# Kernel optimization log

Hardware: AMD Instinct MI355X
Metric: run time of the kernel (lower is better)

Reference implementation:

```python
import jax, jax.numpy as jnp
import numpy as np

NUM_CLASSES = 20
IOU_T = 0.5
NEG_RATIO = 3.0
VXY = 0.1
VWH = 0.2
EPS16 = 9.765625e-4  # torch.finfo(torch.float16).eps


def ltrb2xywh(b):
    return jnp.concatenate([(b[..., :2] + b[..., 2:]) * 0.5, b[..., 2:] - b[..., :2]], -1)


def xywh2ltrb(b):
    return jnp.concatenate([b[..., :2] - b[..., 2:] * 0.5, b[..., :2] + b[..., 2:] * 0.5], -1)


def pairwise_iou(gb, ab):
    # gb [G,4] ltrb, ab [A,4] ltrb -> [G,A]
    lt = jnp.maximum(gb[:, None, :2], ab[None, :, :2])
    rb = jnp.minimum(gb[:, None, 2:], ab[None, :, 2:])
    wh = jnp.clip(rb - lt, 0.0)
    inter = wh[..., 0] * wh[..., 1]
    area_g = (gb[:, 2] - gb[:, 0]) * (gb[:, 3] - gb[:, 1])
    area_a = (ab[:, 2] - ab[:, 0]) * (ab[:, 3] - ab[:, 1])
    return inter / jnp.clip(area_g[:, None] + area_a[None, :] - inter, 1e-8)


def setup_inputs() -> dict:
    key = jax.random.key(0)
    k = jax.random.split(key, 7)
    B, A, G, C = 64, 8732, 50, NUM_CLASSES + 1
    preg = jax.random.normal(k[0], (B, 4, A), jnp.float32) * 0.1
    pcls = jax.random.normal(k[1], (B, C, A), jnp.float32)
    acxy = jax.random.uniform(k[2], (A, 2), jnp.float32)
    awh = jax.random.uniform(k[3], (A, 2), jnp.float32, 0.05, 0.5)
    ancs_xywh = jnp.concatenate([acxy, awh], -1)
    gcxy = jax.random.uniform(k[4], (B, G, 2), jnp.float32, 0.2, 0.8)
    gwh = jax.random.uniform(k[5], (B, G, 2), jnp.float32, 0.05, 0.4)
    gboxes_ltrb = jnp.concatenate([gcxy - gwh * 0.5, gcxy + gwh * 0.5], -1)
    glabels = jax.random.randint(k[6], (B, G), 0, C)  # 0 == padding/background
    return {"preg": preg, "pcls": pcls, "ancs_xywh": ancs_xywh,
            "gboxes_ltrb": gboxes_ltrb, "glabels": glabels}


def _loss(preg, pcls, ancs_xywh, gboxes_ltrb, glabels):
    B, _, A = preg.shape
    preg_bad = jnp.transpose(preg, (0, 2, 1))  # [B,A,4]
    anc_ltrb = xywh2ltrb(ancs_xywh)

    def match(gb, gl):
        iou = pairwise_iou(gb, anc_ltrb)                    # [G,A]
        iou = jnp.where((gl > 0)[:, None], iou, -1.0)       # mask padded gts
        return jnp.argmax(iou, 0), jnp.max(iou, 0) >= IOU_T  # best gt per anchor, pos mask

    boxes_index, mask_pos = jax.vmap(match)(gboxes_ltrb, glabels)  # [B,A],[B,A]

    glabel = jnp.where(mask_pos, jnp.take_along_axis(glabels, boxes_index, 1), 0)  # [B,A]
    gbox_ltrb = jnp.take_along_axis(gboxes_ltrb, boxes_index[..., None], 1)        # [B,A,4]

    gxywh = ltrb2xywh(gbox_ltrb)
    txy = (gxywh[..., :2] - ancs_xywh[None, :, :2]) / (ancs_xywh[None, :, 2:] * VXY)
    twh = jnp.log(jnp.clip(gxywh[..., 2:], 1e-6) / ancs_xywh[None, :, 2:]) / VWH
    gtxywh = jnp.concatenate([txy, twh], -1)
    d = preg_bad - gtxywh
    ad = jnp.abs(d)
    sl1 = jnp.where(ad < 1.0, 0.5 * d * d, ad - 0.5).sum(-1)   # [B,A]
    posf = mask_pos.astype(preg.dtype)
    n_pos_total = jnp.clip(posf.sum(), 1.0)
    l_box = (sl1 * posf).sum() / n_pos_total

    # ---- classification: CE + OHEM hard negatives ----
    logp = jax.nn.log_softmax(pcls, axis=1)                     # [B,C,A]
    ce = -jnp.take_along_axis(logp, glabel[:, None, :], 1)[:, 0, :]  # [B,A]
    nums_pos = jnp.clip(posf.sum(-1), EPS16)                    # [B]

    loss_neg = jnp.where(mask_pos, 0.0, ce)
    order = jnp.argsort(-loss_neg, axis=-1)
    rank = jnp.argsort(order, axis=-1)
    mask_neg = (rank < (NEG_RATIO * nums_pos)[:, None]) & (~mask_pos)
    negf = mask_neg.astype(preg.dtype)

    l_conf_pos = ((ce * posf).sum(-1) / nums_pos).mean()
    l_conf_neg = ((ce * negf).sum(-1) / nums_pos).mean()
    return l_box + l_conf_pos + l_conf_neg


def reference(preg, pcls, ancs_xywh, gboxes_ltrb, glabels):
    return _loss(preg, pcls, ancs_xywh, gboxes_ltrb, glabels)
```

## Files before the change

### kernel.cpp

```cpp
#include <hip/hip_runtime.h>

#define B_ 64
#define A_ 8732
#define G_ 50
#define C_ 21
#define NBF 18
#define NQ 2183
#define NV4 9

__global__ __launch_bounds__(256) void k_fused(
    const float* __restrict__ preg,
    const float* __restrict__ pcls,
    const float* __restrict__ ancs,
    const float* __restrict__ gbox,
    const int*   __restrict__ glab,
    float* __restrict__ loss_neg,
    int*   __restrict__ pos_part,
    float* __restrict__ sl1_part,
    float* __restrict__ cep_part)
{
    __shared__ float redf[8];
    __shared__ int   redi[4];
    __shared__ float4 sbox[G_];
    __shared__ float  sag[G_];
    __shared__ int    slab[G_];
    __shared__ int    snv[1];

    const int b = blockIdx.y, tid = threadIdx.x;
    const int wid = tid >> 6, lane = tid & 63;
    const int pr_i = blockIdx.x * 256 + tid;
    const bool valid = (2 * pr_i) < A_;
    const int a0 = (valid ? pr_i : (A_ / 2 - 1)) * 2;

    if (wid == 0) {
        const bool in_g = (tid < G_);
        const int lb = in_g ? glab[b * G_ + tid] : 0;
        const bool val = in_g && (lb > 0);
        const unsigned long long m = __ballot(val);
        if (val) {
            const int pos = __popcll(m & ((1ull << lane) - 1ull));
            const float4 g4 = *(const float4*)(gbox + b * (G_ * 4) + 4 * tid);
            sbox[pos] = g4;
            sag[pos]  = (g4.z - g4.x) * (g4.w - g4.y);
            slab[pos] = lb;
        }
        if (lane == 0) snv[0] = (int)__popcll(m);
    }

    const float* pc = pcls + b * (C_ * A_) + a0;
    float2 xv[C_];
    #pragma unroll
    for (int c = 0; c < C_; ++c) xv[c] = *(const float2*)(pc + c * A_);

    const float4 ap0 = ((const float4*)ancs)[a0];
    const float4 ap1 = ((const float4*)ancs)[a0 + 1];
    const float al0 = ap0.x - ap0.z * 0.5f, at0 = ap0.y - ap0.w * 0.5f;
    const float ar0 = ap0.x + ap0.z * 0.5f, ab0 = ap0.y + ap0.w * 0.5f;
    const float al1 = ap1.x - ap1.z * 0.5f, at1 = ap1.y - ap1.w * 0.5f;
    const float ar1 = ap1.x + ap1.z * 0.5f, ab1 = ap1.y + ap1.w * 0.5f;
    const float aa0 = (ar0 - al0) * (ab0 - at0);
    const float aa1 = (ar1 - al1) * (ab1 - at1);

    __syncthreads();
    const int nv = snv[0];

    float bin0 = -1.0f, bun0 = 1.0f, bin1 = -1.0f, bun1 = 1.0f;
    int bgi0 = 0, bgi1 = 0;
    for (int g = 0; g < nv; ++g) {
        const float4 g4 = sbox[g];
        const float ag = sag[g];
        const float ix0 = fmaxf(fminf(g4.z, ar0) - fmaxf(g4.x, al0), 0.0f);
        const float iy0 = fmaxf(fminf(g4.w, ab0) - fmaxf(g4.y, at0), 0.0f);
        const float ix1 = fmaxf(fminf(g4.z, ar1) - fmaxf(g4.x, al1), 0.0f);
        const float iy1 = fmaxf(fminf(g4.w, ab1) - fmaxf(g4.y, at1), 0.0f);
        const float in0 = ix0 * iy0, in1 = ix1 * iy1;
        const float un0 = ag + aa0 - in0;
        const float un1 = ag + aa1 - in1;
        if (in0 * bun0 > bin0 * un0) { bin0 = in0; bun0 = un0; bgi0 = g; }
        if (in1 * bun1 > bin1 * un1) { bin1 = in1; bun1 = un1; bgi1 = g; }
    }
    const bool pos0 = valid && (2.0f * bin0 >= bun0);
    const bool pos1 = valid && (2.0f * bin1 >= bun1);

    int lab0 = 0, lab1 = 0;
    float4 g40 = make_float4(0.f, 0.f, 1.f, 1.f), g41 = g40;
    if (pos0) { g40 = sbox[bgi0]; lab0 = slab[bgi0]; }
    if (pos1) { g41 = sbox[bgi1]; lab1 = slab[bgi1]; }

    float s0 = 0.f, s1 = 0.f, xl0 = 0.f, xl1 = 0.f;
    #pragma unroll
    for (int c = 0; c < C_; ++c) {
        s0 += __expf(xv[c].x);
        s1 += __expf(xv[c].y);
        xl0 = (c == lab0) ? xv[c].x : xl0;
        xl1 = (c == lab1) ? xv[c].y : xl1;
    }
    const float ce0 = __logf(s0) - xl0;
    const float ce1 = __logf(s1) - xl1;

    if (valid)
        *(float2*)(loss_neg + b * A_ + a0) =
            make_float2(pos0 ? 0.f : ce0, pos1 ? 0.f : ce1);

    float sl1 = 0.0f, cep = 0.0f; int pcnt = 0;
    const float* pr = preg + b * (4 * A_) + a0;
    if (pos0) {
        const float gcx = (g40.x + g40.z) * 0.5f, gcy = (g40.y + g40.w) * 0.5f;
        const float t0 = (gcx - ap0.x) / (ap0.z * 0.1f);
        const float t1 = (gcy - ap0.y) / (ap0.w * 0.1f);
        const float t2 = __logf(fmaxf(g40.z - g40.x, 1e-6f) / ap0.z) * 5.0f;
        const float t3 = __logf(fmaxf(g40.w - g40.y, 1e-6f) / ap0.w) * 5.0f;
        #pragma unroll
        for (int k = 0; k < 4; ++k) {
            const float tv = (k == 0) ? t0 : (k == 1) ? t1 : (k == 2) ? t2 : t3;
            const float d  = pr[k * A_] - tv;
            const float ad = fabsf(d);
            sl1 += (ad < 1.0f) ? 0.5f * d * d : ad - 0.5f;
        }
        cep += ce0; ++pcnt;
    }
    if (pos1) {
        const float gcx = (g41.x + g41.z) * 0.5f, gcy = (g41.y + g41.w) * 0.5f;
        const float t0 = (gcx - ap1.x) / (ap1.z * 0.1f);
        const float t1 = (gcy - ap1.y) / (ap1.w * 0.1f);
        const float t2 = __logf(fmaxf(g41.z - g41.x, 1e-6f) / ap1.z) * 5.0f;
        const float t3 = __logf(fmaxf(g41.w - g41.y, 1e-6f) / ap1.w) * 5.0f;
        #pragma unroll
        for (int k = 0; k < 4; ++k) {
            const float tv = (k == 0) ? t0 : (k == 1) ? t1 : (k == 2) ? t2 : t3;
            const float d  = pr[k * A_ + 1] - tv;
            const float ad = fabsf(d);
            sl1 += (ad < 1.0f) ? 0.5f * d * d : ad - 0.5f;
        }
        cep += ce1; ++pcnt;
    }

    for (int o = 32; o > 0; o >>= 1) {
        sl1  += __shfl_down(sl1, o);
        cep  += __shfl_down(cep, o);
        pcnt += __shfl_down(pcnt, o);
    }
    if (lane == 0) { redf[wid] = sl1; redf[4 + wid] = cep; redi[wid] = pcnt; }
    __syncthreads();
    if (tid == 0) {
        const int slot = b * NBF + blockIdx.x;
        pos_part[slot] = redi[0] + redi[1] + redi[2] + redi[3];
        sl1_part[slot] = redf[0] + redf[1] + redf[2] + redf[3];
        cep_part[slot] = redf[4] + redf[5] + redf[6] + redf[7];
    }
}

__global__ __launch_bounds__(256) void k_ohem_final(
    const float* __restrict__ loss_neg,
    const int*   __restrict__ pos_part,
    const float* __restrict__ sl1_part,
    const float* __restrict__ cep_part,
    float* __restrict__ out)
{
    __shared__ int   scnt[2][4];
    __shared__ int   sred[4];
    __shared__ float sredf[4];
    __shared__ int   snp[1];
    const int tid = threadIdx.x;
    const int wid = tid >> 6, lane = tid & 63;

    if (blockIdx.x == B_) {
        int tp = 0; float ts = 0.0f;
        for (int j = tid; j < B_ * NBF; j += 256) { tp += pos_part[j]; ts += sl1_part[j]; }
        for (int o = 32; o > 0; o >>= 1) { tp += __shfl_xor(tp, o); ts += __shfl_xor(ts, o); }
        if (lane == 0) { sred[wid] = tp; sredf[wid] = ts; }
        __syncthreads();
        if (tid == 0) {
            const int   np_tot  = sred[0] + sred[1] + sred[2] + sred[3];
            const float sl1_tot = sredf[0] + sredf[1] + sredf[2] + sredf[3];
            atomicAdd(out, sl1_tot / fmaxf((float)np_tot, 1.0f));
        }
        return;
    }
    const int b = blockIdx.x;

    uint4 v[NV4];
    const uint4* src = (const uint4*)(loss_neg + b * A_);
    #pragma unroll
    for (int i = 0; i < NV4; ++i) {
        const int idx = i * 256 + tid;
        v[i] = (idx < NQ) ? src[idx] : make_uint4(0u, 0u, 0u, 0u);
    }

    unsigned mx = 0u;
    #pragma unroll
    for (int i = 0; i < NV4; ++i)
        mx = max(mx, max(max(v[i].x, v[i].y), max(v[i].z, v[i].w)));
    for (int o = 32; o > 0; o >>= 1)
        mx = max(mx, (unsigned)__shfl_xor((int)mx, o));
    if (lane == 0) sred[wid] = (int)mx;

    int np_l = 0; float cep_l = 0.0f;
    if (tid < NBF) { np_l = pos_part[b * NBF + tid]; cep_l = cep_part[b * NBF + tid]; }
    if (wid == 0) {
        for (int o = 32; o > 0; o >>= 1) {
            np_l  += __shfl_xor(np_l, o);
            cep_l += __shfl_xor(cep_l, o);
        }
        if (lane == 0) snp[0] = np_l;
    }
    __syncthreads();
    const unsigned mxall = max(max((unsigned)sred[0], (unsigned)sred[1]),
                               max((unsigned)sred[2], (unsigned)sred[3]));
    const int np = snp[0];

    if (np == 0) {
        if (tid == 0) atomicAdd(out, __uint_as_float(mxall) * 1024.0f * (1.0f / (float)B_));
        return;
    }
    const int K = min(3 * np, A_);

    unsigned thr = 0u;
    int p = 0;
    for (int bit = 30; bit >= 0; --bit) {
        const unsigned cand = thr | (1u << bit);
        if (cand > mxall) continue;
        int c = 0;
        #pragma unroll
        for (int i = 0; i < NV4; ++i) {
            c += __builtin_popcountll(__ballot(v[i].x >= cand));
            c += __builtin_popcountll(__ballot(v[i].y >= cand));
            c += __builtin_popcountll(__ballot(v[i].z >= cand));
            c += __builtin_popcountll(__ballot(v[i].w >= cand));
        }
        if (lane == 0) scnt[p][wid] = c;
        __syncthreads();
        const int tot = scnt[p][0] + scnt[p][1] + scnt[p][2] + scnt[p][3];
        p ^= 1;
        if (tot >= K) thr = cand;
    }

    float ss = 0.0f; int cgt = 0;
    #pragma unroll
    for (int i = 0; i < NV4; ++i) {
        if (v[i].x > thr) { ss += __uint_as_float(v[i].x); ++cgt; }
        if (v[i].y > thr) { ss += __uint_as_float(v[i].y); ++cgt; }
        if (v[i].z > thr) { ss += __uint_as_float(v[i].z); ++cgt; }
        if (v[i].w > thr) { ss += __uint_as_float(v[i].w); ++cgt; }
    }
    for (int o = 32; o > 0; o >>= 1) {
        ss  += __shfl_xor(ss, o);
        cgt += __shfl_xor(cgt, o);
    }
    if (lane == 0) { sredf[wid] = ss; scnt[p][wid] = cgt; }
    __syncthreads();
    if (tid == 0) {
        const float sgt = sredf[0] + sredf[1] + sredf[2] + sredf[3];
        const int   ngt = scnt[p][0] + scnt[p][1] + scnt[p][2] + scnt[p][3];
        const float t = __uint_as_float(thr);
        const float fnp = (float)np;
        const float l_neg = (sgt + (float)(K - ngt) * t) / fnp;
        const float l_pos = cep_l / fnp;
        atomicAdd(out, (l_neg + l_pos) * (1.0f / (float)B_));
    }
}

extern "C" void kernel_launch(void* const* d_in, const int* in_sizes, int n_in,
                              void* d_out, int out_size, void* d_ws, size_t ws_size,
                              hipStream_t stream)
{
    const float* preg = (const float*)d_in[0];
    const float* pcls = (const float*)d_in[1];
    const float* ancs = (const float*)d_in[2];
    const float* gbox = (const float*)d_in[3];
    const int*   glab = (const int*)d_in[4];
    float* out = (float*)d_out;

    float* loss_neg = (float*)d_ws;
    int*   pos_part = (int*)(loss_neg + (size_t)B_ * A_);
    float* sl1_part = (float*)(pos_part + B_ * NBF);
    float* cep_part = sl1_part + B_ * NBF;

    dim3 gF(NBF, B_);
    k_fused<<<gF, 256, 0, stream>>>(preg, pcls, ancs, gbox, glab,
                                    loss_neg, pos_part, sl1_part, cep_part);
    k_ohem_final<<<B_ + 1, 256, 0, stream>>>(loss_neg, pos_part, sl1_part, cep_part, out);
}
```

Baseline: 121.4 us.

## Merge OHEM selection into fused kernel using last-block atomic counters

Folds the second kernel into the first. Per-image atomic counters pick the last finishing block of each image, and that block runs the radix threshold selection and the loss reduction. A global counter then lets the last image add the box-loss term. This removes one kernel launch and the gap between the two kernels, but adds a memset, fences and atomics, and puts the selection tail on a few late blocks.

```diff
diff --git a/kernel.cpp b/kernel.cpp
--- a/kernel.cpp
+++ b/kernel.cpp
@@ -8,7 +8,7 @@
 #define NQ 2183
 #define NV4 9
 
-__global__ __launch_bounds__(256) void k_fused(
+__global__ __launch_bounds__(256) void k_all(
     const float* __restrict__ preg,
     const float* __restrict__ pcls,
     const float* __restrict__ ancs,
@@ -17,7 +17,10 @@
     float* __restrict__ loss_neg,
     int*   __restrict__ pos_part,
     float* __restrict__ sl1_part,
-    float* __restrict__ cep_part)
+    float* __restrict__ cep_part,
+    int*   __restrict__ ctrs,
+    float* __restrict__ gsl1,
+    float* __restrict__ out)
 {
     __shared__ float redf[8];
     __shared__ int   redi[4];
@@ -25,6 +28,11 @@
     __shared__ float  sag[G_];
     __shared__ int    slab[G_];
     __shared__ int    snv[1];
+    __shared__ int    slast[1];
+    __shared__ int    scnt[2][4];
+    __shared__ int    smx[4];
+    __shared__ float  sredf[4];
+    __shared__ int    snp2[1];
 
     const int b = blockIdx.y, tid = threadIdx.x;
     const int wid = tid >> 6, lane = tid & 63;
@@ -148,36 +156,15 @@
         sl1_part[slot] = redf[0] + redf[1] + redf[2] + redf[3];
         cep_part[slot] = redf[4] + redf[5] + redf[6] + redf[7];
     }
-}
-
-__global__ __launch_bounds__(256) void k_ohem_final(
-    const float* __restrict__ loss_neg,
-    const int*   __restrict__ pos_part,
-    const float* __restrict__ sl1_part,
-    const float* __restrict__ cep_part,
-    float* __restrict__ out)
-{
-    __shared__ int   scnt[2][4];
-    __shared__ int   sred[4];
-    __shared__ float sredf[4];
-    __shared__ int   snp[1];
-    const int tid = threadIdx.x;
-    const int wid = tid >> 6, lane = tid & 63;
-
-    if (blockIdx.x == B_) {
-        int tp = 0; float ts = 0.0f;
-        for (int j = tid; j < B_ * NBF; j += 256) { tp += pos_part[j]; ts += sl1_part[j]; }
-        for (int o = 32; o > 0; o >>= 1) { tp += __shfl_xor(tp, o); ts += __shfl_xor(ts, o); }
-        if (lane == 0) { sred[wid] = tp; sredf[wid] = ts; }
-        __syncthreads();
-        if (tid == 0) {
-            const int   np_tot  = sred[0] + sred[1] + sred[2] + sred[3];
-            const float sl1_tot = sredf[0] + sredf[1] + sredf[2] + sredf[3];
-            atomicAdd(out, sl1_tot / fmaxf((float)np_tot, 1.0f));
-        }
-        return;
-    }
-    const int b = blockIdx.x;
+
+    __threadfence();
+    __syncthreads();
+    if (tid == 0)
+        slast[0] = (__hip_atomic_fetch_add(&ctrs[b], 1, __ATOMIC_ACQ_REL,
+                                           __HIP_MEMORY_SCOPE_AGENT) == NBF - 1);
+    __syncthreads();
+    if (!slast[0]) return;
+    __threadfence();
 
     uint4 v[NV4];
     const uint4* src = (const uint4*)(loss_neg + b * A_);
@@ -193,70 +180,90 @@
         mx = max(mx, max(max(v[i].x, v[i].y), max(v[i].z, v[i].w)));
     for (int o = 32; o > 0; o >>= 1)
         mx = max(mx, (unsigned)__shfl_xor((int)mx, o));
-    if (lane == 0) sred[wid] = (int)mx;
-
-    int np_l = 0; float cep_l = 0.0f;
-    if (tid < NBF) { np_l = pos_part[b * NBF + tid]; cep_l = cep_part[b * NBF + tid]; }
+    if (lane == 0) smx[wid] = (int)mx;
+
+    int np_l = 0; float cep_l = 0.0f, sl1_l = 0.0f;
+    if (tid < NBF) {
+        np_l  = pos_part[b * NBF + tid];
+        cep_l = cep_part[b * NBF + tid];
+        sl1_l = sl1_part[b * NBF + tid];
+    }
     if (wid == 0) {
         for (int o = 32; o > 0; o >>= 1) {
             np_l  += __shfl_xor(np_l, o);
             cep_l += __shfl_xor(cep_l, o);
-        }
-        if (lane == 0) snp[0] = np_l;
-    }
-    __syncthreads();
-    const unsigned mxall = max(max((unsigned)sred[0], (unsigned)sred[1]),
-                               max((unsigned)sred[2], (unsigned)sred[3]));
-    const int np = snp[0];
-
+            sl1_l += __shfl_xor(sl1_l, o);
+        }
+        if (lane == 0) snp2[0] = np_l;
+    }
+    __syncthreads();
+    const unsigned mxall = max(max((unsigned)smx[0], (unsigned)smx[1]),
+                               max((unsigned)smx[2], (unsigned)smx[3]));
+    const int np = snp2[0];
+
+    float term = 0.0f;
     if (np == 0) {
-        if (tid == 0) atomicAdd(out, __uint_as_float(mxall) * 1024.0f * (1.0f / (float)B_));
-        return;
-    }
-    const int K = min(3 * np, A_);
-
-    unsigned thr = 0u;
-    int p = 0;
-    for (int bit = 30; bit >= 0; --bit) {
-        const unsigned cand = thr | (1u << bit);
-        if (cand > mxall) continue;
-        int c = 0;
+        term = __uint_as_float(mxall) * 1024.0f * (1.0f / (float)B_);
+    } else {
+        const int K = min(3 * np, A_);
+
+        unsigned thr = 0u;
+        int p = 0;
+        for (int bit = 30; bit >= 0; --bit) {
+            const unsigned cand = thr | (1u << bit);
+            if (cand > mxall) continue;
+            int c = 0;
+            #pragma unroll
+            for (int i = 0; i < NV4; ++i) {
+                c += __builtin_popcountll(__ballot(v[i].x >= cand));
+                c += __builtin_popcountll(__ballot(v[i].y >= cand));
+                c += __builtin_popcountll(__ballot(v[i].z >= cand));
+                c += __builtin_popcountll(__ballot(v[i].w >= cand));
+            }
+            if (lane == 0) scnt[p][wid] = c;
+            __syncthreads();
+            const int tot = scnt[p][0] + scnt[p][1] + scnt[p][2] + scnt[p][3];
+            p ^= 1;
+            if (tot >= K) thr = cand;
+        }
+
+        float ss = 0.0f; int cgt = 0;
         #pragma unroll
         for (int i = 0; i < NV4; ++i) {
-            c += __builtin_popcountll(__ballot(v[i].x >= cand));
-            c += __builtin_popcountll(__ballot(v[i].y >= cand));
-            c += __builtin_popcountll(__ballot(v[i].z >= cand));
-            c += __builtin_popcountll(__ballot(v[i].w >= cand));
-        }
-        if (lane == 0) scnt[p][wid] = c;
+            if (v[i].x > thr) { ss += __uint_as_float(v[i].x); ++cgt; }
+            if (v[i].y > thr) { ss += __uint_as_float(v[i].y); ++cgt; }
+            if (v[i].z > thr) { ss += __uint_as_float(v[i].z); ++cgt; }
+            if (v[i].w > thr) { ss += __uint_as_float(v[i].w); ++cgt; }
+        }
+        for (int o = 32; o > 0; o >>= 1) {
+            ss  += __shfl_xor(ss, o);
+            cgt += __shfl_xor(cgt, o);
+        }
+        if (lane == 0) { sredf[wid] = ss; scnt[p][wid] = cgt; }
         __syncthreads();
-        const int tot = scnt[p][0] + scnt[p][1] + scnt[p][2] + scnt[p][3];
-        p ^= 1;
-        if (tot >= K) thr = cand;
-    }
-
-    float ss = 0.0f; int cgt = 0;
-    #pragma unroll
-    for (int i = 0; i < NV4; ++i) {
-        if (v[i].x > thr) { ss += __uint_as_float(v[i].x); ++cgt; }
-        if (v[i].y > thr) { ss += __uint_as_float(v[i].y); ++cgt; }
-        if (v[i].z > thr) { ss += __uint_as_float(v[i].z); ++cgt; }
-        if (v[i].w > thr) { ss += __uint_as_float(v[i].w); ++cgt; }
-    }
-    for (int o = 32; o > 0; o >>= 1) {
-        ss  += __shfl_xor(ss, o);
-        cgt += __shfl_xor(cgt, o);
-    }
-    if (lane == 0) { sredf[wid] = ss; scnt[p][wid] = cgt; }
-    __syncthreads();
+        if (tid == 0) {
+            const float sgt = sredf[0] + sredf[1] + sredf[2] + sredf[3];
+            const int   ngt = scnt[p][0] + scnt[p][1] + scnt[p][2] + scnt[p][3];
+            const float t = __uint_as_float(thr);
+            const float fnp = (float)np;
+            term = ((sgt + (float)(K - ngt) * t) / fnp + cep_l / fnp) * (1.0f / (float)B_);
+        }
+    }
+
     if (tid == 0) {
-        const float sgt = sredf[0] + sredf[1] + sredf[2] + sredf[3];
-        const int   ngt = scnt[p][0] + scnt[p][1] + scnt[p][2] + scnt[p][3];
-        const float t = __uint_as_float(thr);
-        const float fnp = (float)np;
-        const float l_neg = (sgt + (float)(K - ngt) * t) / fnp;
-        const float l_pos = cep_l / fnp;
-        atomicAdd(out, (l_neg + l_pos) * (1.0f / (float)B_));
+        atomicAdd(out, term);
+        atomicAdd(&ctrs[B_ + 1], np);
+        atomicAdd(gsl1, sl1_l);
+        __threadfence();
+        const int o2 = __hip_atomic_fetch_add(&ctrs[B_], 1, __ATOMIC_ACQ_REL,
+                                              __HIP_MEMORY_SCOPE_AGENT);
+        if (o2 == B_ - 1) {
+            const int   np_tot  = __hip_atomic_load(&ctrs[B_ + 1], __ATOMIC_ACQUIRE,
+                                                    __HIP_MEMORY_SCOPE_AGENT);
+            const float sl1_tot = __hip_atomic_load(gsl1, __ATOMIC_ACQUIRE,
+                                                    __HIP_MEMORY_SCOPE_AGENT);
+            atomicAdd(out, sl1_tot / fmaxf((float)np_tot, 1.0f));
+        }
     }
 }
 
@@ -275,9 +282,13 @@
     int*   pos_part = (int*)(loss_neg + (size_t)B_ * A_);
     float* sl1_part = (float*)(pos_part + B_ * NBF);
     float* cep_part = sl1_part + B_ * NBF;
+    int*   ctrs     = (int*)(cep_part + B_ * NBF);
+    float* gsl1     = (float*)(ctrs + B_ + 2);
+
+    hipMemsetAsync(ctrs, 0, (B_ + 3) * sizeof(int), stream);
 
     dim3 gF(NBF, B_);
-    k_fused<<<gF, 256, 0, stream>>>(preg, pcls, ancs, gbox, glab,
-                                    loss_neg, pos_part, sl1_part, cep_part);
-    k_ohem_final<<<B_ + 1, 256, 0, stream>>>(loss_neg, pos_part, sl1_part, cep_part, out);
+    k_all<<<gF, 256, 0, stream>>>(preg, pcls, ancs, gbox, glab,
+                                  loss_neg, pos_part, sl1_part, cep_part,
+                                  ctrs, gsl1, out);
 }
```

Result: slower. 277.2 us (+128.4%).
